# Optimization experiments

Measured on AMD Instinct MI355X. Metric: run time of the kernel, lower is better.

The kernel has to match this reference:

```python
import jax, jax.numpy as jnp
import numpy as np

D_MODEL = 1024
N_HEADS = 16
HEAD_DIM = D_MODEL // N_HEADS
FF_DIM = 1024  # repo bug: linear2 is Linear(d_model, ff_dim); ff_dim==d_model required for residual
EPS = 1e-5


def _linear_params(k, d_in, d_out):
    kw, kb = jax.random.split(k)
    bound = 1.0 / np.sqrt(d_in)
    W = jax.random.uniform(kw, (d_out, d_in), minval=-bound, maxval=bound, dtype=jnp.float32)
    b = jax.random.uniform(kb, (d_out,), minval=-bound, maxval=bound, dtype=jnp.float32)
    return W, b


def setup_inputs() -> dict:
    key = jax.random.key(0)
    ks = jax.random.split(key, 8)
    src = jax.random.normal(ks[0], (4, 2048, D_MODEL), dtype=jnp.float32)
    Wq, bq = _linear_params(ks[1], D_MODEL, D_MODEL)
    Wk, bk = _linear_params(ks[2], D_MODEL, D_MODEL)
    Wv, bv = _linear_params(ks[3], D_MODEL, D_MODEL)
    Wo, bo = _linear_params(ks[4], D_MODEL, D_MODEL)
    W1, b1 = _linear_params(ks[5], D_MODEL, FF_DIM)
    W2, b2 = _linear_params(ks[6], D_MODEL, FF_DIM)
    g1 = jnp.ones((D_MODEL,), jnp.float32); be1 = jnp.zeros((D_MODEL,), jnp.float32)
    g2 = jnp.ones((D_MODEL,), jnp.float32); be2 = jnp.zeros((D_MODEL,), jnp.float32)
    return {"src": src, "Wq": Wq, "bq": bq, "Wk": Wk, "bk": bk, "Wv": Wv, "bv": bv,
            "Wo": Wo, "bo": bo, "W1": W1, "b1": b1, "W2": W2, "b2": b2,
            "g1": g1, "be1": be1, "g2": g2, "be2": be2}


def _layernorm(x, g, b):
    mu = jnp.mean(x, axis=-1, keepdims=True)
    var = jnp.var(x, axis=-1, keepdims=True)
    return (x - mu) * jax.lax.rsqrt(var + EPS) * g + b


def _mha(x, Wq, bq, Wk, bk, Wv, bv, Wo, bo):
    B, S, _ = x.shape
    def proj(W, b):
        return (x @ W.T + b).reshape(B, S, N_HEADS, HEAD_DIM).transpose(0, 2, 1, 3)
    Q, K, V = proj(Wq, bq), proj(Wk, bk), proj(Wv, bv)
    scale = jnp.float32(np.sqrt(HEAD_DIM))
    energy = jnp.einsum('bhqd,bhkd->bhqk', Q, K) / scale
    attn = jax.nn.softmax(energy, axis=-1)
    out = jnp.einsum('bhqk,bhkd->bhqd', attn, V)
    out = out.transpose(0, 2, 1, 3).reshape(B, S, D_MODEL)
    return out @ Wo.T + bo


def reference(src, Wq, bq, Wk, bk, Wv, bv, Wo, bo, W1, b1, W2, b2, g1, be1, g2, be2):
    x = src
    x = x + _mha(_layernorm(x, g1, be1), Wq, bq, Wk, bk, Wv, bv, Wo, bo)
    h = _layernorm(x, g2, be2)
    ff = jax.nn.relu(h @ W1.T + b1) @ W2.T + b2
    return x + ff
```

## Files before the change

### kernel.cpp

```cpp
#include <hip/hip_runtime.h>
#include <stdint.h>

typedef __attribute__((ext_vector_type(8))) short    bf16x8;
typedef __attribute__((ext_vector_type(4))) short    bf16x4;
typedef __attribute__((ext_vector_type(4))) float    f32x4;
typedef __attribute__((ext_vector_type(8))) uint16_t u16x8;
typedef __attribute__((ext_vector_type(4))) uint16_t u16x4;

#define D_MODEL 1024
#define SEQ     2048
#define NB      4
#define NH      16
#define HD      64
#define MTOK    8192

__device__ __forceinline__ float bf2f(uint16_t u) {
    union { uint32_t i; float f; } x; x.i = ((uint32_t)u) << 16; return x.f;
}
__device__ __forceinline__ uint16_t f2bf(float f) {
    union { float f; uint32_t i; } x; x.f = f;
    uint32_t r = (x.i + 0x7fffu + ((x.i >> 16) & 1u)) >> 16;
    return (uint16_t)r;
}
__device__ __forceinline__ void gload16(const void* g, void* l) {
    __builtin_amdgcn_global_load_lds(
        (const __attribute__((address_space(1))) unsigned int*)g,
        (__attribute__((address_space(3))) unsigned int*)l, 16, 0, 0);
}
__device__ __forceinline__ bf16x8 lds_ld8(const uint16_t* p) {
    bf16x4 a = *(const bf16x4*)p;
    bf16x4 b = *(const bf16x4*)(p + 4);
    bf16x8 r;
    r[0] = a[0]; r[1] = a[1]; r[2] = a[2]; r[3] = a[3];
    r[4] = b[0]; r[5] = b[1]; r[6] = b[2]; r[7] = b[3];
    return r;
}
__device__ __forceinline__ uint32_t pk_bf16_trunc(float lo, float hi) {
    return __builtin_amdgcn_perm(__float_as_uint(hi), __float_as_uint(lo), 0x07060302u);
}

__global__ __launch_bounds__(256)
void cvt_all(const float* __restrict__ s0, const float* __restrict__ s1,
             const float* __restrict__ s2, const float* __restrict__ s3,
             const float* __restrict__ s4, const float* __restrict__ s5,
             uint16_t* __restrict__ dQKV, uint16_t* __restrict__ dWo,
             uint16_t* __restrict__ dW1, uint16_t* __restrict__ dW2)
{
    const float* srcs[6] = {s0, s1, s2, s3, s4, s5};
    uint16_t* dsts[6] = {dQKV, dQKV + (size_t)D_MODEL * D_MODEL,
                         dQKV + 2 * (size_t)D_MODEL * D_MODEL, dWo, dW1, dW2};
    const float* in = srcs[blockIdx.y];
    uint16_t* out = dsts[blockIdx.y];
    const int i = (blockIdx.x * 256 + threadIdx.x) * 4;
    float4 v = *(const float4*)(in + i);
    u16x4 o;
    o[0] = f2bf(v.x); o[1] = f2bf(v.y); o[2] = f2bf(v.z); o[3] = f2bf(v.w);
    *(u16x4*)(out + i) = o;
}

__global__ __launch_bounds__(256)
void ln_kernel(const float* __restrict__ x, const float* __restrict__ g,
               const float* __restrict__ be, uint16_t* __restrict__ y)
{
    const int row = blockIdx.x;
    const int tid = threadIdx.x;
    const size_t base = (size_t)row * D_MODEL + tid * 4;
    float4 v = *(const float4*)(x + base);
    float f[4] = {v.x, v.y, v.z, v.w};
    float sum = 0.f, sq = 0.f;
#pragma unroll
    for (int e = 0; e < 4; e++) { sum += f[e]; sq += f[e] * f[e]; }
#pragma unroll
    for (int o = 32; o > 0; o >>= 1) { sum += __shfl_down(sum, o); sq += __shfl_down(sq, o); }
    __shared__ float ps[4], pq[4];
    const int lane = tid & 63, wid = tid >> 6;
    if (lane == 0) { ps[wid] = sum; pq[wid] = sq; }
    __syncthreads();
    const float ts = ps[0] + ps[1] + ps[2] + ps[3];
    const float tq = pq[0] + pq[1] + pq[2] + pq[3];
    const float mean = ts * (1.0f / D_MODEL);
    const float var  = tq * (1.0f / D_MODEL) - mean * mean;
    const float rstd = rsqrtf(var + 1e-5f);
    float4 gv = *(const float4*)(g + tid * 4);
    float4 bv = *(const float4*)(be + tid * 4);
    const float gg[4] = {gv.x, gv.y, gv.z, gv.w};
    const float bb[4] = {bv.x, bv.y, bv.z, bv.w};
    u16x4 outv;
#pragma unroll
    for (int e = 0; e < 4; e++)
        outv[e] = f2bf((f[e] - mean) * rstd * gg[e] + bb[e]);
    *(u16x4*)(y + base) = outv;
}

template<int RESID, int RELU, int OUTF32>
__global__ __launch_bounds__(256, 3)
void gemm_bt128(const uint16_t* __restrict__ A, const uint16_t* __restrict__ W,
                const float* __restrict__ bias, const float* __restrict__ resid,
                void* __restrict__ Cv)
{
    __shared__ uint16_t lA[128 * 32];
    __shared__ uint16_t lB[128 * 32];
    const int tid  = threadIdx.x;
    const int lane = tid & 63;
    const int quad = lane >> 4;
    const int l16  = lane & 15;
    const int wid  = tid >> 6;
    const int wm   = wid >> 1;
    const int wn   = wid & 1;
    const int m0   = blockIdx.y * 128;
    const int n0   = blockIdx.x * 128;

    f32x4 acc[4][4];
#pragma unroll
    for (int i = 0; i < 4; i++)
#pragma unroll
        for (int j = 0; j < 4; j++) acc[i][j] = (f32x4){0.f, 0.f, 0.f, 0.f};

    const int sr = tid >> 2;
    const int sc = (tid & 3) * 8;
    const uint16_t* gA0 = A + (size_t)(m0 + sr) * D_MODEL + sc;
    const uint16_t* gA1 = gA0 + (size_t)64 * D_MODEL;
    const uint16_t* gW0 = W + (size_t)(n0 + sr) * D_MODEL + sc;
    const uint16_t* gW1 = gW0 + (size_t)64 * D_MODEL;
    uint16_t* sA0 = &lA[tid * 8];
    uint16_t* sA1 = sA0 + 2048;
    uint16_t* sB0 = &lB[tid * 8];
    uint16_t* sB1 = sB0 + 2048;

    for (int k0 = 0; k0 < D_MODEL; k0 += 32) {
        __syncthreads();
        gload16(gA0 + k0, sA0);
        gload16(gA1 + k0, sA1);
        gload16(gW0 + k0, sB0);
        gload16(gW1 + k0, sB1);
        __syncthreads();
        bf16x8 fa[4], fb[4];
#pragma unroll
        for (int i = 0; i < 4; i++)
            fa[i] = *(const bf16x8*)&lA[(wm * 64 + i * 16 + l16) * 32 + quad * 8];
#pragma unroll
        for (int j = 0; j < 4; j++)
            fb[j] = *(const bf16x8*)&lB[(wn * 64 + j * 16 + l16) * 32 + quad * 8];
#pragma unroll
        for (int i = 0; i < 4; i++)
#pragma unroll
            for (int j = 0; j < 4; j++)
                acc[i][j] = __builtin_amdgcn_mfma_f32_16x16x32_bf16(fa[i], fb[j], acc[i][j], 0, 0, 0);
    }

#pragma unroll
    for (int j = 0; j < 4; j++) {
        const int col = n0 + wn * 64 + j * 16 + l16;
        const float bvv = bias[col];
#pragma unroll
        for (int i = 0; i < 4; i++) {
            const int row = m0 + wm * 64 + i * 16 + quad * 4;
#pragma unroll
            for (int r = 0; r < 4; r++) {
                float v = acc[i][j][r] + bvv;
                const size_t idx = (size_t)(row + r) * D_MODEL + col;
                if (RESID) v += resid[idx];
                if (RELU)  v = fmaxf(v, 0.0f);
                if (OUTF32) ((float*)Cv)[idx] = v;
                else        ((uint16_t*)Cv)[idx] = f2bf(v);
            }
        }
    }
}

#define QSCALE 0.18033688f
__global__ __launch_bounds__(256, 3)
void gemm_qkv(const uint16_t* __restrict__ A, const uint16_t* __restrict__ Wqkv,
              const float* __restrict__ bq, const float* __restrict__ bk,
              const float* __restrict__ bv, uint16_t* __restrict__ Qb,
              uint16_t* __restrict__ Kb, uint16_t* __restrict__ Vt)
{
    __shared__ uint16_t lA[128 * 32];
    __shared__ uint16_t lB[128 * 32];
    const int tid  = threadIdx.x;
    const int lane = tid & 63;
    const int quad = lane >> 4;
    const int l16  = lane & 15;
    const int wid  = tid >> 6;
    const int wm   = wid >> 1;
    const int wn   = wid & 1;
    const int t0   = blockIdx.y * 128;
    const int n0   = blockIdx.x * 128;
    const int which = n0 >> 10;
    const int lc0   = n0 & 1023;

    f32x4 acc[4][4];
#pragma unroll
    for (int i = 0; i < 4; i++)
#pragma unroll
        for (int j = 0; j < 4; j++) acc[i][j] = (f32x4){0.f, 0.f, 0.f, 0.f};

    const int sr = tid >> 2;
    const int sc = (tid & 3) * 8;
    const uint16_t* gA0 = A + (size_t)(t0 + sr) * D_MODEL + sc;
    const uint16_t* gA1 = gA0 + (size_t)64 * D_MODEL;
    const uint16_t* gW0 = Wqkv + (size_t)(n0 + sr) * D_MODEL + sc;
    const uint16_t* gW1 = gW0 + (size_t)64 * D_MODEL;
    uint16_t* sA0 = &lA[tid * 8];
    uint16_t* sA1 = sA0 + 2048;
    uint16_t* sB0 = &lB[tid * 8];
    uint16_t* sB1 = sB0 + 2048;

    for (int k0 = 0; k0 < D_MODEL; k0 += 32) {
        __syncthreads();
        gload16(gA0 + k0, sA0);
        gload16(gA1 + k0, sA1);
        gload16(gW0 + k0, sB0);
        gload16(gW1 + k0, sB1);
        __syncthreads();
        bf16x8 fa[4], fb[4];
        if (which != 2) {
#pragma unroll
            for (int i = 0; i < 4; i++)
                fa[i] = *(const bf16x8*)&lA[(wm * 64 + i * 16 + l16) * 32 + quad * 8];
#pragma unroll
            for (int j = 0; j < 4; j++)
                fb[j] = *(const bf16x8*)&lB[(wn * 64 + j * 16 + l16) * 32 + quad * 8];
        } else {
#pragma unroll
            for (int i = 0; i < 4; i++)
                fa[i] = *(const bf16x8*)&lB[(wm * 64 + i * 16 + l16) * 32 + quad * 8];
#pragma unroll
            for (int j = 0; j < 4; j++)
                fb[j] = *(const bf16x8*)&lA[(wn * 64 + j * 16 + l16) * 32 + quad * 8];
        }
#pragma unroll
        for (int i = 0; i < 4; i++)
#pragma unroll
            for (int j = 0; j < 4; j++)
                acc[i][j] = __builtin_amdgcn_mfma_f32_16x16x32_bf16(fa[i], fb[j], acc[i][j], 0, 0, 0);
    }

    if (which != 2) {
        const float* bias = (which == 0) ? bq : bk;
        uint16_t* C = (which == 0) ? Qb : Kb;
        const float alpha = (which == 0) ? QSCALE : 1.0f;
#pragma unroll
        for (int j = 0; j < 4; j++) {
            const int col = lc0 + wn * 64 + j * 16 + l16;
            const float bvv = bias[col];
#pragma unroll
            for (int i = 0; i < 4; i++) {
                const int row = t0 + wm * 64 + i * 16 + quad * 4;
#pragma unroll
                for (int r = 0; r < 4; r++)
                    C[(size_t)(row + r) * D_MODEL + col] = f2bf((acc[i][j][r] + bvv) * alpha);
            }
        }
    } else {
#pragma unroll
        for (int i = 0; i < 4; i++) {
#pragma unroll
            for (int r = 0; r < 4; r++) {
                const int wrow = lc0 + wm * 64 + i * 16 + quad * 4 + r;
                const float bvv = bv[wrow];
#pragma unroll
                for (int j = 0; j < 4; j++) {
                    const int tok = t0 + wn * 64 + j * 16 + l16;
                    Vt[(size_t)wrow * MTOK + tok] = f2bf(acc[i][j][r] + bvv);
                }
            }
        }
    }
}

#define PST 68
__global__ __launch_bounds__(256, 4)
void attn_kernel(const uint16_t* __restrict__ Q, const uint16_t* __restrict__ K,
                 const uint16_t* __restrict__ Vt, uint16_t* __restrict__ O)
{
    __shared__ uint16_t sQP[128 * PST];
    __shared__ uint16_t sK [64 * PST];
    __shared__ uint16_t sVt[64 * PST];
    __shared__ float    sSt[128];

    const int tid  = threadIdx.x;
    const int lane = tid & 63;
    const int quad = lane >> 4;
    const int l16  = lane & 15;
    const int w    = tid >> 6;

    const int bh = blockIdx.x;
    const int h  = bh & (NH - 1);
    const int b  = bh >> 4;
    const int q0 = blockIdx.y * 128;
    const size_t headoff = (size_t)h * HD;
    const size_t bbase   = (size_t)b * SEQ;

    const int r8 = tid >> 3;
    const int c8 = (tid & 7) * 8;

#pragma unroll
    for (int i = 0; i < 4; i++)
        gload16(Q + (bbase + q0 + i * 32 + r8) * D_MODEL + headoff + c8, &sQP[i * 2048 + tid * 8]);
    __syncthreads();

    bf16x8 qa[2][2];
#pragma unroll
    for (int i = 0; i < 2; i++)
#pragma unroll
        for (int ks = 0; ks < 2; ks++)
            qa[i][ks] = *(const bf16x8*)&sQP[(w * 32 + i * 16 + l16) * 64 + ks * 32 + quad * 8];

    f32x4 oacc[2][4];
#pragma unroll
    for (int i = 0; i < 2; i++)
#pragma unroll
        for (int n = 0; n < 4; n++) oacc[i][n] = (f32x4){0.f, 0.f, 0.f, 0.f};
    float lrun[2] = {0.f, 0.f};

    const uint16_t* gK  = K  + bbase * D_MODEL + headoff;
    const uint16_t* gVt = Vt + headoff * MTOK + bbase;

    u16x8 kreg[2], vreg[2];
#pragma unroll
    for (int i = 0; i < 2; i++) {
        const int row = i * 32 + r8;
        kreg[i] = *(const u16x8*)(gK + (size_t)row * D_MODEL + c8);
        vreg[i] = *(const u16x8*)(gVt + (size_t)row * MTOK + c8);
    }

    for (int kv0 = 0; kv0 < SEQ; kv0 += 64) {
        __syncthreads();
#pragma unroll
        for (int i = 0; i < 2; i++) {
            const int row = i * 32 + r8;
            *(u16x4*)&sK [(size_t)row * PST + c8]     = (u16x4){kreg[i][0], kreg[i][1], kreg[i][2], kreg[i][3]};
            *(u16x4*)&sK [(size_t)row * PST + c8 + 4] = (u16x4){kreg[i][4], kreg[i][5], kreg[i][6], kreg[i][7]};
            *(u16x4*)&sVt[(size_t)row * PST + c8]     = (u16x4){vreg[i][0], vreg[i][1], vreg[i][2], vreg[i][3]};
            *(u16x4*)&sVt[(size_t)row * PST + c8 + 4] = (u16x4){vreg[i][4], vreg[i][5], vreg[i][6], vreg[i][7]};
        }
        __syncthreads();

        if (kv0 + 64 < SEQ) {
            const int kvn = kv0 + 64;
#pragma unroll
            for (int i = 0; i < 2; i++) {
                const int row = i * 32 + r8;
                kreg[i] = *(const u16x8*)(gK + (size_t)(kvn + row) * D_MODEL + c8);
                vreg[i] = *(const u16x8*)(gVt + (size_t)row * MTOK + kvn + c8);
            }
        }

        f32x4 st[4][2];
#pragma unroll
        for (int j = 0; j < 4; j++)
#pragma unroll
            for (int i = 0; i < 2; i++) st[j][i] = (f32x4){0.f, 0.f, 0.f, 0.f};
#pragma unroll
        for (int ks = 0; ks < 2; ks++)
#pragma unroll
            for (int j = 0; j < 4; j++) {
                bf16x8 kb = lds_ld8(&sK[(j * 16 + l16) * PST + ks * 32 + quad * 8]);
#pragma unroll
                for (int i = 0; i < 2; i++)
                    st[j][i] = __builtin_amdgcn_mfma_f32_16x16x32_bf16(kb, qa[i][ks], st[j][i], 0, 0, 0);
            }

#pragma unroll
        for (int i = 0; i < 2; i++) {
            float rs = 0.f;
#pragma unroll
            for (int j = 0; j < 4; j++) {
#pragma unroll
                for (int r = 0; r < 4; r++) {
                    const float p = __builtin_amdgcn_exp2f(st[j][i][r]);
                    st[j][i][r] = p;
                    rs += p;
                }
            }
            lrun[i] += rs;
#pragma unroll
            for (int j = 0; j < 4; j++) {
                uint2 pk;
                pk.x = pk_bf16_trunc(st[j][i][0], st[j][i][1]);
                pk.y = pk_bf16_trunc(st[j][i][2], st[j][i][3]);
                *(uint2*)&sQP[(size_t)(w * 32 + i * 16 + l16) * PST + j * 16 + quad * 4] = pk;
            }
        }

#pragma unroll
        for (int i = 0; i < 2; i++)
#pragma unroll
            for (int ks = 0; ks < 2; ks++) {
                bf16x8 pa = lds_ld8(&sQP[(size_t)(w * 32 + i * 16 + l16) * PST + ks * 32 + quad * 8]);
#pragma unroll
                for (int n = 0; n < 4; n++) {
                    bf16x8 vb = lds_ld8(&sVt[(n * 16 + l16) * PST + ks * 32 + quad * 8]);
                    oacc[i][n] = __builtin_amdgcn_mfma_f32_16x16x32_bf16(pa, vb, oacc[i][n], 0, 0, 0);
                }
            }
    }

#pragma unroll
    for (int i = 0; i < 2; i++) {
        lrun[i] += __shfl_xor(lrun[i], 16);
        lrun[i] += __shfl_xor(lrun[i], 32);
        sSt[w * 32 + i * 16 + l16] = 1.0f / lrun[i];
    }
#pragma unroll
    for (int i = 0; i < 2; i++)
#pragma unroll
        for (int r = 0; r < 4; r++) {
            const size_t row = bbase + q0 + w * 32 + i * 16 + quad * 4 + r;
            const float inv = sSt[w * 32 + i * 16 + quad * 4 + r];
#pragma unroll
            for (int n = 0; n < 4; n++)
                O[row * D_MODEL + headoff + n * 16 + l16] = f2bf(oacc[i][n][r] * inv);
        }
}

extern "C" void kernel_launch(void* const* d_in, const int* in_sizes, int n_in,
                              void* d_out, int out_size, void* d_ws, size_t ws_size,
                              hipStream_t stream)
{
    const float* src = (const float*)d_in[0];
    const float* Wq  = (const float*)d_in[1];
    const float* bq  = (const float*)d_in[2];
    const float* Wk  = (const float*)d_in[3];
    const float* bk  = (const float*)d_in[4];
    const float* Wv  = (const float*)d_in[5];
    const float* bv  = (const float*)d_in[6];
    const float* Wo  = (const float*)d_in[7];
    const float* bo  = (const float*)d_in[8];
    const float* W1  = (const float*)d_in[9];
    const float* b1  = (const float*)d_in[10];
    const float* W2  = (const float*)d_in[11];
    const float* b2  = (const float*)d_in[12];
    const float* g1  = (const float*)d_in[13];
    const float* be1 = (const float*)d_in[14];
    const float* g2  = (const float*)d_in[15];
    const float* be2 = (const float*)d_in[16];
    float* out = (float*)d_out;

    uint16_t* ws  = (uint16_t*)d_ws;
    const size_t BUF = (size_t)MTOK * D_MODEL;
    const size_t WSZ = (size_t)D_MODEL * D_MODEL;
    uint16_t* xn1  = ws;
    uint16_t* Vtb  = ws + BUF;
    uint16_t* wQKV = ws + 2 * BUF;
    uint16_t* wWo  = wQKV + 3 * WSZ;
    uint16_t* wW1  = wWo + WSZ;
    uint16_t* wW2  = wW1 + WSZ;
    uint16_t* Qb   = (uint16_t*)d_out;
    uint16_t* Kb   = Qb + BUF;
    float*    x2   = (float*)d_out;

    dim3 blk(256);
    cvt_all<<<dim3(1024, 6), 256, 0, stream>>>(Wq, Wk, Wv, Wo, W1, W2, wQKV, wWo, wW1, wW2);
    ln_kernel<<<8192, 256, 0, stream>>>(src, g1, be1, xn1);
    gemm_qkv<<<dim3(24, 64), blk, 0, stream>>>(xn1, wQKV, bq, bk, bv, Qb, Kb, Vtb);
    attn_kernel<<<dim3(64, 16), 256, 0, stream>>>(Qb, Kb, Vtb, xn1);
    gemm_bt128<1, 0, 1><<<dim3(8, 64), blk, 0, stream>>>(xn1, wWo, bo, src, x2);
    ln_kernel<<<8192, 256, 0, stream>>>(x2, g2, be2, xn1);
    gemm_bt128<0, 1, 0><<<dim3(8, 64), blk, 0, stream>>>(xn1, wW1, b1, nullptr, Vtb);
    gemm_bt128<1, 0, 1><<<dim3(8, 64), blk, 0, stream>>>(Vtb, wW2, b2, x2, out);
}
```

Before: 398.4 us.

## Double-buffer LDS in projection GEMMs and drop attention register prefetch

The two bf16 GEMM kernels (generic and fused QKV) now use two LDS buffers. The next 32-wide K slice is loaded while the current one is computed, which cuts the loop to one barrier per slice and overlaps global-to-LDS copies with MFMA work. The attention kernel stops prefetching the next K/V tile into registers and instead loads each tile at the top of its iteration, which frees registers but exposes the load latency. Doubling LDS per block (32 KB) may lower occupancy under the 3-blocks-per-CU launch bound.

```diff
diff --git a/kernel.cpp b/kernel.cpp
--- a/kernel.cpp
+++ b/kernel.cpp
@@ -98,8 +98,8 @@
                 const float* __restrict__ bias, const float* __restrict__ resid,
                 void* __restrict__ Cv)
 {
-    __shared__ uint16_t lA[128 * 32];
-    __shared__ uint16_t lB[128 * 32];
+    __shared__ uint16_t lA[2][128 * 32];
+    __shared__ uint16_t lB[2][128 * 32];
     const int tid  = threadIdx.x;
     const int lane = tid & 63;
     const int quad = lane >> 4;
@@ -122,31 +122,41 @@
     const uint16_t* gA1 = gA0 + (size_t)64 * D_MODEL;
     const uint16_t* gW0 = W + (size_t)(n0 + sr) * D_MODEL + sc;
     const uint16_t* gW1 = gW0 + (size_t)64 * D_MODEL;
-    uint16_t* sA0 = &lA[tid * 8];
-    uint16_t* sA1 = sA0 + 2048;
-    uint16_t* sB0 = &lB[tid * 8];
-    uint16_t* sB1 = sB0 + 2048;
-
-    for (int k0 = 0; k0 < D_MODEL; k0 += 32) {
-        __syncthreads();
-        gload16(gA0 + k0, sA0);
-        gload16(gA1 + k0, sA1);
-        gload16(gW0 + k0, sB0);
-        gload16(gW1 + k0, sB1);
-        __syncthreads();
-        bf16x8 fa[4], fb[4];
-#pragma unroll
-        for (int i = 0; i < 4; i++)
-            fa[i] = *(const bf16x8*)&lA[(wm * 64 + i * 16 + l16) * 32 + quad * 8];
-#pragma unroll
-        for (int j = 0; j < 4; j++)
-            fb[j] = *(const bf16x8*)&lB[(wn * 64 + j * 16 + l16) * 32 + quad * 8];
-#pragma unroll
-        for (int i = 0; i < 4; i++)
-#pragma unroll
-            for (int j = 0; j < 4; j++)
-                acc[i][j] = __builtin_amdgcn_mfma_f32_16x16x32_bf16(fa[i], fb[j], acc[i][j], 0, 0, 0);
-    }
+
+    #define STAGE_BT(k0, b) do {                      \
+        gload16(gA0 + (k0), &lA[b][tid * 8]);         \
+        gload16(gA1 + (k0), &lA[b][2048 + tid * 8]);  \
+        gload16(gW0 + (k0), &lB[b][tid * 8]);         \
+        gload16(gW1 + (k0), &lB[b][2048 + tid * 8]);  \
+    } while (0)
+
+    #define COMP_BT(b) do {                                                           \
+        bf16x8 fa[4], fb[4];                                                          \
+        _Pragma("unroll")                                                             \
+        for (int i = 0; i < 4; i++)                                                   \
+            fa[i] = *(const bf16x8*)&lA[b][(wm * 64 + i * 16 + l16) * 32 + quad * 8]; \
+        _Pragma("unroll")                                                             \
+        for (int j = 0; j < 4; j++)                                                   \
+            fb[j] = *(const bf16x8*)&lB[b][(wn * 64 + j * 16 + l16) * 32 + quad * 8]; \
+        _Pragma("unroll")                                                             \
+        for (int i = 0; i < 4; i++)                                                   \
+            _Pragma("unroll")                                                         \
+            for (int j = 0; j < 4; j++)                                               \
+                acc[i][j] = __builtin_amdgcn_mfma_f32_16x16x32_bf16(fa[i], fb[j], acc[i][j], 0, 0, 0); \
+    } while (0)
+
+    STAGE_BT(0, 0);
+    __syncthreads();
+    for (int k0 = 0; k0 < D_MODEL; k0 += 64) {
+        STAGE_BT(k0 + 32, 1);
+        COMP_BT(0);
+        __syncthreads();
+        if (k0 + 64 < D_MODEL) STAGE_BT(k0 + 64, 0);
+        COMP_BT(1);
+        __syncthreads();
+    }
+    #undef STAGE_BT
+    #undef COMP_BT
 
 #pragma unroll
     for (int j = 0; j < 4; j++) {
@@ -175,8 +185,8 @@
               const float* __restrict__ bv, uint16_t* __restrict__ Qb,
               uint16_t* __restrict__ Kb, uint16_t* __restrict__ Vt)
 {
-    __shared__ uint16_t lA[128 * 32];
-    __shared__ uint16_t lB[128 * 32];
+    __shared__ uint16_t lA[2][128 * 32];
+    __shared__ uint16_t lB[2][128 * 32];
     const int tid  = threadIdx.x;
     const int lane = tid & 63;
     const int quad = lane >> 4;
@@ -201,40 +211,50 @@
     const uint16_t* gA1 = gA0 + (size_t)64 * D_MODEL;
     const uint16_t* gW0 = Wqkv + (size_t)(n0 + sr) * D_MODEL + sc;
     const uint16_t* gW1 = gW0 + (size_t)64 * D_MODEL;
-    uint16_t* sA0 = &lA[tid * 8];
-    uint16_t* sA1 = sA0 + 2048;
-    uint16_t* sB0 = &lB[tid * 8];
-    uint16_t* sB1 = sB0 + 2048;
-
-    for (int k0 = 0; k0 < D_MODEL; k0 += 32) {
-        __syncthreads();
-        gload16(gA0 + k0, sA0);
-        gload16(gA1 + k0, sA1);
-        gload16(gW0 + k0, sB0);
-        gload16(gW1 + k0, sB1);
-        __syncthreads();
-        bf16x8 fa[4], fb[4];
-        if (which != 2) {
-#pragma unroll
-            for (int i = 0; i < 4; i++)
-                fa[i] = *(const bf16x8*)&lA[(wm * 64 + i * 16 + l16) * 32 + quad * 8];
-#pragma unroll
-            for (int j = 0; j < 4; j++)
-                fb[j] = *(const bf16x8*)&lB[(wn * 64 + j * 16 + l16) * 32 + quad * 8];
-        } else {
-#pragma unroll
-            for (int i = 0; i < 4; i++)
-                fa[i] = *(const bf16x8*)&lB[(wm * 64 + i * 16 + l16) * 32 + quad * 8];
-#pragma unroll
-            for (int j = 0; j < 4; j++)
-                fb[j] = *(const bf16x8*)&lA[(wn * 64 + j * 16 + l16) * 32 + quad * 8];
-        }
-#pragma unroll
-        for (int i = 0; i < 4; i++)
-#pragma unroll
-            for (int j = 0; j < 4; j++)
-                acc[i][j] = __builtin_amdgcn_mfma_f32_16x16x32_bf16(fa[i], fb[j], acc[i][j], 0, 0, 0);
-    }
+
+    #define STAGE_QKV(k0, b) do {                     \
+        gload16(gA0 + (k0), &lA[b][tid * 8]);         \
+        gload16(gA1 + (k0), &lA[b][2048 + tid * 8]);  \
+        gload16(gW0 + (k0), &lB[b][tid * 8]);         \
+        gload16(gW1 + (k0), &lB[b][2048 + tid * 8]);  \
+    } while (0)
+
+    #define COMP_QKV(b) do {                                                              \
+        bf16x8 fa[4], fb[4];                                                              \
+        if (which != 2) {                                                                 \
+            _Pragma("unroll")                                                             \
+            for (int i = 0; i < 4; i++)                                                   \
+                fa[i] = *(const bf16x8*)&lA[b][(wm * 64 + i * 16 + l16) * 32 + quad * 8]; \
+            _Pragma("unroll")                                                             \
+            for (int j = 0; j < 4; j++)                                                   \
+                fb[j] = *(const bf16x8*)&lB[b][(wn * 64 + j * 16 + l16) * 32 + quad * 8]; \
+        } else {                                                                          \
+            _Pragma("unroll")                                                             \
+            for (int i = 0; i < 4; i++)                                                   \
+                fa[i] = *(const bf16x8*)&lB[b][(wm * 64 + i * 16 + l16) * 32 + quad * 8]; \
+            _Pragma("unroll")                                                             \
+            for (int j = 0; j < 4; j++)                                                   \
+                fb[j] = *(const bf16x8*)&lA[b][(wn * 64 + j * 16 + l16) * 32 + quad * 8]; \
+        }                                                                                 \
+        _Pragma("unroll")                                                                 \
+        for (int i = 0; i < 4; i++)                                                       \
+            _Pragma("unroll")                                                             \
+            for (int j = 0; j < 4; j++)                                                   \
+                acc[i][j] = __builtin_amdgcn_mfma_f32_16x16x32_bf16(fa[i], fb[j], acc[i][j], 0, 0, 0); \
+    } while (0)
+
+    STAGE_QKV(0, 0);
+    __syncthreads();
+    for (int k0 = 0; k0 < D_MODEL; k0 += 64) {
+        STAGE_QKV(k0 + 32, 1);
+        COMP_QKV(0);
+        __syncthreads();
+        if (k0 + 64 < D_MODEL) STAGE_QKV(k0 + 64, 0);
+        COMP_QKV(1);
+        __syncthreads();
+    }
+    #undef STAGE_QKV
+    #undef COMP_QKV
 
     if (which != 2) {
         const float* bias = (which == 0) ? bq : bk;
@@ -317,15 +337,14 @@
     const uint16_t* gK  = K  + bbase * D_MODEL + headoff;
     const uint16_t* gVt = Vt + headoff * MTOK + bbase;
 
-    u16x8 kreg[2], vreg[2];
-#pragma unroll
-    for (int i = 0; i < 2; i++) {
-        const int row = i * 32 + r8;
-        kreg[i] = *(const u16x8*)(gK + (size_t)row * D_MODEL + c8);
-        vreg[i] = *(const u16x8*)(gVt + (size_t)row * MTOK + c8);
-    }
-
     for (int kv0 = 0; kv0 < SEQ; kv0 += 64) {
+        u16x8 kreg[2], vreg[2];
+#pragma unroll
+        for (int i = 0; i < 2; i++) {
+            const int row = i * 32 + r8;
+            kreg[i] = *(const u16x8*)(gK + (size_t)(kv0 + row) * D_MODEL + c8);
+            vreg[i] = *(const u16x8*)(gVt + (size_t)row * MTOK + kv0 + c8);
+        }
         __syncthreads();
 #pragma unroll
         for (int i = 0; i < 2; i++) {
@@ -336,16 +355,6 @@
             *(u16x4*)&sVt[(size_t)row * PST + c8 + 4] = (u16x4){vreg[i][4], vreg[i][5], vreg[i][6], vreg[i][7]};
         }
         __syncthreads();
-
-        if (kv0 + 64 < SEQ) {
-            const int kvn = kv0 + 64;
-#pragma unroll
-            for (int i = 0; i < 2; i++) {
-                const int row = i * 32 + r8;
-                kreg[i] = *(const u16x8*)(gK + (size_t)(kvn + row) * D_MODEL + c8);
-                vreg[i] = *(const u16x8*)(gVt + (size_t)row * MTOK + kvn + c8);
-            }
-        }
 
         f32x4 st[4][2];
 #pragma unroll
```

New measurement: 400.8 us. About the same (+0.6%).
